# Kernel optimization log

Hardware: AMD Instinct MI355X
Metric: run time of the kernel (lower is better)

Reference implementation:

```python
import jax, jax.numpy as jnp
import numpy as np

EMBED_DIM = 1024
NUM_HEADS = 16
DK = EMBED_DIM // NUM_HEADS  # 64
B, S = 8, 4096


def setup_inputs() -> dict:
    key = jax.random.key(0)
    ks = jax.random.split(key, 7)
    init = 1.0 / np.sqrt(EMBED_DIM)
    x = jax.random.normal(ks[0], (B, S, EMBED_DIM), dtype=jnp.float32)
    Wq = jax.random.uniform(ks[1], (EMBED_DIM, EMBED_DIM), jnp.float32, -init, init)
    bq = jax.random.uniform(ks[2], (EMBED_DIM,), jnp.float32, -init, init)
    Wk = jax.random.uniform(ks[3], (EMBED_DIM, EMBED_DIM), jnp.float32, -init, init)
    bk = jax.random.uniform(ks[4], (EMBED_DIM,), jnp.float32, -init, init)
    Wv = jax.random.uniform(ks[5], (EMBED_DIM, EMBED_DIM), jnp.float32, -init, init)
    bv = jax.random.uniform(ks[6], (EMBED_DIM,), jnp.float32, -init, init)
    return {"x": x, "Wq": Wq, "bq": bq, "Wk": Wk, "bk": bk, "Wv": Wv, "bv": bv}


def reference(x, Wq, bq, Wk, bk, Wv, bv):
    batch_size, seq_length, _ = x.shape
    # Linear projections (torch nn.Linear: x @ W.T + b)
    q = x @ Wq.T + bq  # [B, S, E]
    k = x @ Wk.T + bk
    v = x @ Wv.T + bv
    scaling = 1.0 / jnp.sqrt(jnp.asarray(DK, dtype=x.dtype))
    # Faithful to original: transpose(1,2) then reshape splits heads along the
    # embedding axis -> per-head tensors of shape [B*H, dk, S]
    q = jnp.transpose(q, (0, 2, 1)).reshape(batch_size * NUM_HEADS, DK, seq_length)
    k = jnp.transpose(k, (0, 2, 1)).reshape(batch_size * NUM_HEADS, DK, seq_length)
    k = jnp.transpose(k, (0, 2, 1))  # [B*H, S, dk]
    v = jnp.transpose(v, (0, 2, 1)).reshape(batch_size * NUM_HEADS, DK, seq_length)
    # attn: [B*H, dk, dk] -- attention over channel dims (as in the original code)
    attn = jax.nn.softmax(jnp.einsum('bds,bse->bde', q, k) * scaling, axis=-1)
    output = jnp.einsum('bde,bes->bds', attn, v)  # [B*H, dk, S]
    output = output.reshape(batch_size, EMBED_DIM, seq_length)
    return jnp.transpose(output, (0, 2, 1))  # [B, S, E]
```

## Files before the change

### kernel.cpp

```cpp
#include <hip/hip_runtime.h>
#include <hip/hip_bf16.h>
#include <stdint.h>


#define B_   8
#define S_   4096
#define E_   1024
#define H_   16
#define NSPLIT 4

typedef float floatx4 __attribute__((ext_vector_type(4)));
typedef short short8  __attribute__((ext_vector_type(8)));

#define MFMA(a,b,c) __builtin_amdgcn_mfma_f32_16x16x32_bf16((a),(b),(c),0,0,0)

static __device__ __forceinline__ unsigned short f2bf(float x){
    __hip_bfloat16 h = __float2bfloat16(x);
    return __builtin_bit_cast(unsigned short, h);
}
static __device__ __forceinline__ float bf2f(unsigned short u){
    unsigned int w = ((unsigned int)u) << 16;
    return __builtin_bit_cast(float, w);
}
static __device__ __forceinline__ short8 lds_load8(const unsigned short* p) {
    union { ushort4 u4[2]; short8 s8; } f;
    f.u4[0] = *(const ushort4*)(p);
    f.u4[1] = *(const ushort4*)(p + 4);
    return f.s8;
}
static __device__ __forceinline__ int swz(int chunk, int row){
    return chunk ^ ((row >> 3) & 7) ^ (row & 7);
}
static __device__ __forceinline__ int rk_idx(int row, int col){
    return row * 128 + (((col >> 3) ^ (row & 15)) << 3) + (col & 7);
}
#define SWIZ(row, q) ((q) ^ (((row) >> 1) & 3))

__global__ __launch_bounds__(256) void sums_kernel(
    const float* __restrict__ X, float* __restrict__ cpart, float* __restrict__ d2part)
{
    const int b = blockIdx.y, chunk = blockIdx.z;
    const int e = blockIdx.x * 256 + threadIdx.x;
    const float* p = X + ((size_t)b * S_ + chunk * 256) * E_ + e;
    float s1 = 0.f, s2 = 0.f;
#pragma unroll 8
    for (int i = 0; i < 256; ++i) {
        float v = p[(size_t)i * E_];
        s1 += v; s2 += v * v;
    }
    cpart [(chunk * B_ + b) * E_ + e] = s1;
    d2part[(chunk * B_ + b) * E_ + e] = s2;
}

__global__ __launch_bounds__(256) void reduce_kernel(
    const float* __restrict__ cpart, const float* __restrict__ d2part,
    float* __restrict__ c, float* __restrict__ gdiag)
{
    const int idx = blockIdx.x * 256 + threadIdx.x;
    const int b = idx >> 10, e = idx & 1023;
    float s1 = 0.f, s2 = 0.f;
#pragma unroll
    for (int p = 0; p < 16; ++p) {
        s1 += cpart [(p * B_ + b) * E_ + e];
        s2 += d2part[(p * B_ + b) * E_ + e];
    }
    c[idx] = s1; gdiag[idx] = s2;
}

__global__ __launch_bounds__(256) void uqk_kernel(
    const float* __restrict__ Wq, const float* __restrict__ Wk,
    const float* __restrict__ c, float* __restrict__ uq, float* __restrict__ uk)
{
    const int b = blockIdx.y;
    const int j = blockIdx.x * 256 + threadIdx.x;
    const float* cb = c + b * E_;
    const float* q = Wq + (size_t)j * E_;
    const float* k = Wk + (size_t)j * E_;
    float sq = 0.f, sk = 0.f;
    for (int i = 0; i < E_; i += 4) {
        float4 vq = *(const float4*)(q + i);
        float4 vk = *(const float4*)(k + i);
        float4 cv = *(const float4*)(cb + i);
        sq += vq.x*cv.x + vq.y*cv.y + vq.z*cv.z + vq.w*cv.w;
        sk += vk.x*cv.x + vk.y*cv.y + vk.z*cv.z + vk.w*cv.w;
    }
    uq[b * E_ + j] = sq;
    uk[b * E_ + j] = sk;
}

__global__ __launch_bounds__(256, 4) void gram_kernel(
    const float* __restrict__ X, float* __restrict__ Gp)
{
    const int b = blockIdx.y;
    const int ks = blockIdx.z;
    int u = blockIdx.x, mb = 0;
    while (u >= 8 - mb) { u -= 8 - mb; ++mb; }
    const int nb = mb + u;
    const int m0 = mb * 128, n0 = nb * 128;
    const bool diag = (mb == nb);
    const int t = threadIdx.x, lane = t & 63, w = t >> 6;
    const int l15 = lane & 15, quad = lane >> 4;
    const int mw = 64 * (w >> 1), nw = 64 * (w & 1);
    const int e4 = t & 31, sgrp = t >> 5;

    __shared__ __align__(16) unsigned short At[128 * 64];
    __shared__ __align__(16) unsigned short Bt[128 * 64];

    const floatx4 fz = {0.f, 0.f, 0.f, 0.f};
    floatx4 acc[4][4];
#pragma unroll
    for (int i = 0; i < 4; ++i)
#pragma unroll
        for (int j = 0; j < 4; ++j) acc[i][j] = fz;

    const float* Xb = X + (size_t)b * S_ * E_;
    const int s_begin = ks * (S_ / NSPLIT);
    const int s_end   = s_begin + (S_ / NSPLIT);

    for (int s0 = s_begin; s0 < s_end; s0 += 64) {
        __syncthreads();
#pragma unroll
        for (int p = 0; p < 2; ++p) {
            float4 va[4], vb[4];
#pragma unroll
            for (int i = 0; i < 4; ++i) {
                const int sl = 8 * sgrp + 4 * p + i;
                va[i] = *(const float4*)(Xb + (size_t)(s0 + sl) * E_ + m0 + e4 * 4);
                if (!diag)
                    vb[i] = *(const float4*)(Xb + (size_t)(s0 + sl) * E_ + n0 + e4 * 4);
            }
#pragma unroll
            for (int j = 0; j < 4; ++j) {
                const int e = e4 * 4 + j;
                ushort4 wa;
                wa.x = f2bf(((const float*)&va[0])[j]);
                wa.y = f2bf(((const float*)&va[1])[j]);
                wa.z = f2bf(((const float*)&va[2])[j]);
                wa.w = f2bf(((const float*)&va[3])[j]);
                *(ushort4*)&At[e * 64 + swz(sgrp, e) * 8 + 4 * p] = wa;
                if (!diag) {
                    ushort4 wb;
                    wb.x = f2bf(((const float*)&vb[0])[j]);
                    wb.y = f2bf(((const float*)&vb[1])[j]);
                    wb.z = f2bf(((const float*)&vb[2])[j]);
                    wb.w = f2bf(((const float*)&vb[3])[j]);
                    *(ushort4*)&Bt[e * 64 + swz(sgrp, e) * 8 + 4 * p] = wb;
                }
            }
        }
        __syncthreads();
        const unsigned short* Bp = diag ? At : Bt;
#pragma unroll
        for (int kk = 0; kk < 2; ++kk) {
            const int q = kk * 4 + quad;
            short8 af[4], bfr[4];
#pragma unroll
            for (int i = 0; i < 4; ++i) {
                const int row = mw + 16 * i + l15;
                af[i] = lds_load8(&At[row * 64 + swz(q, row) * 8]);
            }
#pragma unroll
            for (int j = 0; j < 4; ++j) {
                const int row = nw + 16 * j + l15;
                bfr[j] = lds_load8(&Bp[row * 64 + swz(q, row) * 8]);
            }
#pragma unroll
            for (int i = 0; i < 4; ++i)
#pragma unroll
                for (int j = 0; j < 4; ++j)
                    acc[i][j] = MFMA(af[i], bfr[j], acc[i][j]);
        }
    }

    float* Gb = Gp + ((size_t)ks * B_ + b) * E_ * E_;
#pragma unroll
    for (int jt = 0; jt < 4; ++jt)
#pragma unroll
        for (int i = 0; i < 4; ++i)
#pragma unroll
            for (int r = 0; r < 4; ++r) {
                const int row = mw + 16 * i + quad * 4 + r;
                const int col = nw + 16 * jt + l15;
                const float v = acc[i][jt][r];
                Gb[(size_t)(m0 + row) * E_ + n0 + col] = v;
                if (!diag) Gb[(size_t)(n0 + col) * E_ + m0 + row] = v;
            }
}

__global__ __launch_bounds__(256) void greduce_kernel(float* __restrict__ Gp)
{
    const size_t n = (size_t)B_ * E_ * E_;
    const size_t i = ((size_t)blockIdx.x * 256 + threadIdx.x) * 4;
    float4 v0 = *(const float4*)(Gp + i);
    float4 v1 = *(const float4*)(Gp + n + i);
    float4 v2 = *(const float4*)(Gp + 2 * n + i);
    float4 v3 = *(const float4*)(Gp + 3 * n + i);
    float4 r = { v0.x + v1.x + v2.x + v3.x,
                 v0.y + v1.y + v2.y + v3.y,
                 v0.z + v1.z + v2.z + v3.z,
                 v0.w + v1.w + v2.w + v3.w };
    *(float4*)(Gp + i) = r;
}

__global__ __launch_bounds__(256) void z_kernel(
    const float* __restrict__ G, const float* __restrict__ WqF,
    const float* __restrict__ gdiag, float* __restrict__ Z)
{
    const int b = blockIdx.z;
    const int n0 = blockIdx.x * 128;
    const int m0 = blockIdx.y * 128;
    const int t = threadIdx.x, lane = t & 63, w = t >> 6;
    const int l15 = lane & 15, quad = lane >> 4;
    const int mw = 64 * (w >> 1), nw = 64 * (w & 1);

    __shared__ __align__(16) unsigned short As[128 * 32];
    __shared__ __align__(16) unsigned short Bs[128 * 32];

    const float* Gb = G + (size_t)b * E_ * E_;
    const float* gd = gdiag + b * E_;
    float* Zb = Z + (size_t)b * E_ * E_;

    const floatx4 fz = {0.f, 0.f, 0.f, 0.f};
    floatx4 acc[4][4];
#pragma unroll
    for (int i = 0; i < 4; ++i)
#pragma unroll
        for (int j = 0; j < 4; ++j) acc[i][j] = fz;

    for (int k0 = 0; k0 < E_; k0 += 32) {
        __syncthreads();
#pragma unroll
        for (int it = 0; it < 4; ++it) {
            const int l = t + 256 * it;
            const int c4 = l & 7, row = l >> 3;
            float4 v = *(const float4*)(WqF + (size_t)(m0 + row) * E_ + k0 + c4 * 4);
            ushort4 o = { f2bf(v.x), f2bf(v.y), f2bf(v.z), f2bf(v.w) };
            *(ushort4*)&As[row * 32 + SWIZ(row, c4 >> 1) * 8 + (c4 & 1) * 4] = o;
        }
#pragma unroll
        for (int it = 0; it < 4; ++it) {
            const int l = t + 256 * it;
            const int c4 = l & 7, row = l >> 3;
            const int n = n0 + row;
            float4 v = *(const float4*)(Gb + (size_t)n * E_ + k0 + c4 * 4);
            float vv[4] = {v.x, v.y, v.z, v.w};
            const int dj = n - (k0 + c4 * 4);
            if (dj >= 0 && dj < 4) vv[dj] = 0.f;
            ushort4 o = { f2bf(vv[0]), f2bf(vv[1]), f2bf(vv[2]), f2bf(vv[3]) };
            *(ushort4*)&Bs[row * 32 + SWIZ(row, c4 >> 1) * 8 + (c4 & 1) * 4] = o;
        }
        __syncthreads();
        short8 af[4], bfr[4];
#pragma unroll
        for (int i = 0; i < 4; ++i) {
            const int row = mw + 16 * i + l15;
            af[i] = lds_load8(&As[row * 32 + SWIZ(row, quad) * 8]);
        }
#pragma unroll
        for (int j = 0; j < 4; ++j) {
            const int row = nw + 16 * j + l15;
            bfr[j] = lds_load8(&Bs[row * 32 + SWIZ(row, quad) * 8]);
        }
#pragma unroll
        for (int i = 0; i < 4; ++i)
#pragma unroll
            for (int j = 0; j < 4; ++j)
                acc[i][j] = MFMA(af[i], bfr[j], acc[i][j]);
    }

#pragma unroll
    for (int jt = 0; jt < 4; ++jt) {
        const int n = n0 + nw + 16 * jt + l15;
        const float g = gd[n];
#pragma unroll
        for (int i = 0; i < 4; ++i)
#pragma unroll
            for (int r = 0; r < 4; ++r) {
                const int m = m0 + mw + 16 * i + quad * 4 + r;
                Zb[(size_t)m * E_ + n] = acc[i][jt][r] + WqF[(size_t)m * E_ + n] * g;
            }
    }
}

__global__ __launch_bounds__(256) void attn_kernel(
    const float* __restrict__ Z,
    const float* __restrict__ bqF,
    const float* __restrict__ WkF, const float* __restrict__ bkF,
    const float* __restrict__ WvF, const float* __restrict__ bvF,
    const float* __restrict__ uq, const float* __restrict__ uk,
    unsigned short* __restrict__ Wo, float* __restrict__ bo)
{
    const int bh = blockIdx.x, b = bh >> 4, h = bh & 15;
    const int t = threadIdx.x, lane = t & 63, w = t >> 6;
    const int l15 = lane & 15, quad = lane >> 4;

    __shared__ __align__(16) unsigned char smem[65536];
    unsigned short* ZH  = (unsigned short*)(smem);
    unsigned short* ZL  = (unsigned short*)(smem + 16384);
    unsigned short* KH  = (unsigned short*)(smem + 32768);
    unsigned short* KL  = (unsigned short*)(smem + 49152);
    unsigned short* PB  = (unsigned short*)(smem);
    unsigned short* WVT = (unsigned short*)(smem + 16384);

    const float* Zh  = Z   + ((size_t)b * E_ + h * 64) * E_;
    const float* Wkh = WkF + (size_t)(h * 64) * E_;
    const float* Wvh = WvF + (size_t)(h * 64) * E_;

    const floatx4 fz = {0.f, 0.f, 0.f, 0.f};
    floatx4 lacc[4] = {fz, fz, fz, fz};

    for (int ic = 0; ic < 8; ++ic) {
        __syncthreads();
#pragma unroll
        for (int it = 0; it < 8; ++it) {
            const int l = t + 256 * it;
            const int c4 = l & 31, row = l >> 5;
            float4 v = *(const float4*)(Zh + (size_t)row * E_ + ic * 128 + c4 * 4);
            const float vv[4] = {v.x, v.y, v.z, v.w};
            ushort4 ohi, olo;
#pragma unroll
            for (int j = 0; j < 4; ++j) {
                const unsigned short hi = f2bf(vv[j]);
                ((unsigned short*)&ohi)[j] = hi;
                ((unsigned short*)&olo)[j] = f2bf(vv[j] - bf2f(hi));
            }
            const int off = row * 128 + (((c4 >> 1) ^ (row & 15)) << 3) + (c4 & 1) * 4;
            *(ushort4*)&ZH[off] = ohi;
            *(ushort4*)&ZL[off] = olo;
        }
#pragma unroll
        for (int it = 0; it < 8; ++it) {
            const int l = t + 256 * it;
            const int c4 = l & 31, row = l >> 5;
            float4 v = *(const float4*)(Wkh + (size_t)row * E_ + ic * 128 + c4 * 4);
            const float vv[4] = {v.x, v.y, v.z, v.w};
            ushort4 ohi, olo;
#pragma unroll
            for (int j = 0; j < 4; ++j) {
                const unsigned short hi = f2bf(vv[j]);
                ((unsigned short*)&ohi)[j] = hi;
                ((unsigned short*)&olo)[j] = f2bf(vv[j] - bf2f(hi));
            }
            const int off = row * 128 + (((c4 >> 1) ^ (row & 15)) << 3) + (c4 & 1) * 4;
            *(ushort4*)&KH[off] = ohi;
            *(ushort4*)&KL[off] = olo;
        }
        __syncthreads();
#pragma unroll
        for (int ks = 0; ks < 4; ++ks) {
            const short8 ah = lds_load8(&ZH[rk_idx(16 * w + l15, ks * 32 + quad * 8)]);
            const short8 al = lds_load8(&ZL[rk_idx(16 * w + l15, ks * 32 + quad * 8)]);
#pragma unroll
            for (int jt = 0; jt < 4; ++jt) {
                const short8 bh_ = lds_load8(&KH[rk_idx(16 * jt + l15, ks * 32 + quad * 8)]);
                const short8 bl_ = lds_load8(&KL[rk_idx(16 * jt + l15, ks * 32 + quad * 8)]);
                lacc[jt] = MFMA(ah, bh_, lacc[jt]);
                lacc[jt] = MFMA(ah, bl_, lacc[jt]);
                lacc[jt] = MFMA(al, bh_, lacc[jt]);
            }
        }
    }

    float ukv[4], bkv[4];
#pragma unroll
    for (int jt = 0; jt < 4; ++jt) {
        const int he = h * 64 + 16 * jt + l15;
        ukv[jt] = uk[b * E_ + he];
        bkv[jt] = bkF[he];
    }
    float L[4][4];
#pragma unroll
    for (int r = 0; r < 4; ++r) {
        const int hd = h * 64 + 16 * w + quad * 4 + r;
        const float uqr = uq[b * E_ + hd];
        const float bqr = bqF[hd];
#pragma unroll
        for (int jt = 0; jt < 4; ++jt)
            L[jt][r] = 0.125f * (lacc[jt][r] + bqr * ukv[jt] + bkv[jt] * uqr
                                 + 4096.f * bqr * bkv[jt]);
    }
#pragma unroll
    for (int r = 0; r < 4; ++r) {
        float m = fmaxf(fmaxf(L[0][r], L[1][r]), fmaxf(L[2][r], L[3][r]));
#pragma unroll
        for (int mask = 1; mask < 16; mask <<= 1) m = fmaxf(m, __shfl_xor(m, mask, 64));
        float s = 0.f;
#pragma unroll
        for (int jt = 0; jt < 4; ++jt) { L[jt][r] = __expf(L[jt][r] - m); s += L[jt][r]; }
#pragma unroll
        for (int mask = 1; mask < 16; mask <<= 1) s += __shfl_xor(s, mask, 64);
        const float inv = 1.f / s;
#pragma unroll
        for (int jt = 0; jt < 4; ++jt) L[jt][r] *= inv;
    }

    __syncthreads();
#pragma unroll
    for (int jt = 0; jt < 4; ++jt)
#pragma unroll
        for (int r = 0; r < 4; ++r)
            PB[(16 * w + quad * 4 + r) * 72 + 16 * jt + l15] = f2bf(L[jt][r]);
    __syncthreads();

    if (t < 64) {
        float s = 0.f;
        for (int e = 0; e < 64; ++e) s += bf2f(PB[t * 72 + e]) * bvF[h * 64 + e];
        bo[b * E_ + h * 64 + t] = s;
    }

    unsigned short* Wob = Wo + (size_t)b * E_ * E_;
    for (int nc = 0; nc < 16; ++nc) {
        __syncthreads();
#pragma unroll
        for (int it = 0; it < 4; ++it) {
            const int l = t + 256 * it;
            const int n4 = l & 15, e = l >> 4;
            float4 v = *(const float4*)(Wvh + (size_t)e * E_ + nc * 64 + n4 * 4);
            const float vv[4] = {v.x, v.y, v.z, v.w};
#pragma unroll
            for (int j = 0; j < 4; ++j) {
                const int n = n4 * 4 + j;
                WVT[n * 64 + swz(e >> 3, n) * 8 + (e & 7)] = f2bf(vv[j]);
            }
        }
        __syncthreads();
        floatx4 oacc[4] = {fz, fz, fz, fz};
#pragma unroll
        for (int ks = 0; ks < 2; ++ks) {
            const short8 a = lds_load8(&PB[(16 * w + l15) * 72 + ks * 32 + quad * 8]);
            const int q = ks * 4 + quad;
#pragma unroll
            for (int jt = 0; jt < 4; ++jt) {
                const int row = 16 * jt + l15;
                const short8 bb = lds_load8(&WVT[row * 64 + swz(q, row) * 8]);
                oacc[jt] = MFMA(a, bb, oacc[jt]);
            }
        }
#pragma unroll
        for (int jt = 0; jt < 4; ++jt)
#pragma unroll
            for (int r = 0; r < 4; ++r)
                Wob[(size_t)(h * 64 + 16 * w + quad * 4 + r) * E_ + nc * 64 + 16 * jt + l15]
                    = f2bf(oacc[jt][r]);
    }
}

__global__ __launch_bounds__(256) void out_gemm_kernel(
    const float* __restrict__ X, const unsigned short* __restrict__ Wo,
    const float* __restrict__ bo, float* __restrict__ Out)
{
    const int b = blockIdx.z;
    const int n0 = blockIdx.x * 128;
    const int m0 = blockIdx.y * 128;
    const int t = threadIdx.x, lane = t & 63, w = t >> 6;
    const int l15 = lane & 15, quad = lane >> 4;
    const int mw = 64 * (w >> 1), nw = 64 * (w & 1);

    __shared__ __align__(16) unsigned short As[128 * 32];
    __shared__ __align__(16) unsigned short Bs[128 * 32];

    const float* Xb = X + (size_t)b * S_ * E_;
    const unsigned short* Wb = Wo + (size_t)b * E_ * E_;
    const float* bob = bo + b * E_;
    float* Ob = Out + (size_t)b * S_ * E_;

    const floatx4 fz = {0.f, 0.f, 0.f, 0.f};
    floatx4 acc[4][4];
#pragma unroll
    for (int i = 0; i < 4; ++i)
#pragma unroll
        for (int j = 0; j < 4; ++j) acc[i][j] = fz;

    for (int k0 = 0; k0 < E_; k0 += 32) {
        __syncthreads();
#pragma unroll
        for (int it = 0; it < 4; ++it) {
            const int l = t + 256 * it;
            const int c4 = l & 7, row = l >> 3;
            float4 v = *(const float4*)(Xb + (size_t)(m0 + row) * E_ + k0 + c4 * 4);
            ushort4 o = { f2bf(v.x), f2bf(v.y), f2bf(v.z), f2bf(v.w) };
            *(ushort4*)&As[row * 32 + SWIZ(row, c4 >> 1) * 8 + (c4 & 1) * 4] = o;
        }
#pragma unroll
        for (int it = 0; it < 2; ++it) {
            const int l = t + 256 * it;
            const int ch = l & 3, row = l >> 2;
            uint4 v = *(const uint4*)(Wb + (size_t)(n0 + row) * E_ + k0 + ch * 8);
            *(uint4*)&Bs[row * 32 + SWIZ(row, ch) * 8] = v;
        }
        __syncthreads();
        short8 af[4], bfr[4];
#pragma unroll
        for (int i = 0; i < 4; ++i) {
            const int row = mw + 16 * i + l15;
            af[i] = lds_load8(&As[row * 32 + SWIZ(row, quad) * 8]);
        }
#pragma unroll
        for (int j = 0; j < 4; ++j) {
            const int row = nw + 16 * j + l15;
            bfr[j] = lds_load8(&Bs[row * 32 + SWIZ(row, quad) * 8]);
        }
#pragma unroll
        for (int i = 0; i < 4; ++i)
#pragma unroll
            for (int j = 0; j < 4; ++j)
                acc[i][j] = MFMA(af[i], bfr[j], acc[i][j]);
    }

#pragma unroll
    for (int jt = 0; jt < 4; ++jt) {
        const int n = n0 + nw + 16 * jt + l15;
        const float bv_ = bob[n];
        float* colp = Ob + n;
#pragma unroll
        for (int i = 0; i < 4; ++i)
#pragma unroll
            for (int r = 0; r < 4; ++r) {
                const int m = m0 + mw + 16 * i + quad * 4 + r;
                colp[(size_t)m * E_] = acc[i][jt][r] + bv_;
            }
    }
}

extern "C" void kernel_launch(void* const* d_in, const int* in_sizes, int n_in,
                              void* d_out, int out_size, void* d_ws, size_t ws_size,
                              hipStream_t stream) {
    (void)in_sizes; (void)n_in; (void)out_size; (void)ws_size;
    const float* x  = (const float*)d_in[0];
    const float* Wq = (const float*)d_in[1];
    const float* bq = (const float*)d_in[2];
    const float* Wk = (const float*)d_in[3];
    const float* bk = (const float*)d_in[4];
    const float* Wv = (const float*)d_in[5];
    const float* bv = (const float*)d_in[6];

    unsigned short* Wo = (unsigned short*)d_ws;
    float* cpart  = (float*)(Wo + (size_t)B_ * E_ * E_);
    float* d2part = cpart  + 16 * B_ * E_;
    float* c      = d2part + 16 * B_ * E_;
    float* gdiag  = c      + B_ * E_;
    float* uq     = gdiag  + B_ * E_;
    float* uk     = uq     + B_ * E_;
    float* bo     = uk     + B_ * E_;

    float* Gp = (float*)d_out;
    float* G  = Gp;
    float* Z  = Gp + (size_t)B_ * E_ * E_;

    sums_kernel<<<dim3(4, 8, 16), 256, 0, stream>>>(x, cpart, d2part);
    reduce_kernel<<<dim3(32), 256, 0, stream>>>(cpart, d2part, c, gdiag);
    uqk_kernel<<<dim3(4, 8), 256, 0, stream>>>(Wq, Wk, c, uq, uk);
    gram_kernel<<<dim3(36, 8, NSPLIT), 256, 0, stream>>>(x, Gp);
    greduce_kernel<<<dim3(8192), 256, 0, stream>>>(Gp);
    z_kernel<<<dim3(8, 8, 8), 256, 0, stream>>>(G, Wq, gdiag, Z);
    attn_kernel<<<dim3(128), 256, 0, stream>>>(Z, bq, Wk, bk, Wv, bv,
                                               uq, uk, Wo, bo);
    out_gemm_kernel<<<dim3(8, 32, 8), 256, 0, stream>>>(x, Wo, bo, (float*)d_out);
}
```

Measured before the change: 765.9 us.

## Add register prefetch pipelining and XCD-aware block remapping across GEMM kernels

The gram kernel switches to a 32-wide K step with double-buffered LDS and register prefetch of the next X tile, so global loads overlap the MFMA work. The z and attn kernels gain the same prefetch of the next tile into registers. The gram, z and out_gemm launches become 1D grids, with block ids remapped so that blocks sharing a batch land on the same XCD for L2 locality. The costs are higher register pressure (gram launch bounds drop to 3 blocks per CU) and more LDS in gram.

```diff
diff --git a/kernel.cpp b/kernel.cpp
--- a/kernel.cpp
+++ b/kernel.cpp
@@ -35,6 +35,7 @@
     return row * 128 + (((col >> 3) ^ (row & 15)) << 3) + (col & 7);
 }
 #define SWIZ(row, q) ((q) ^ (((row) >> 1) & 3))
+#define GSWZ(row, q) ((q) ^ (((row) >> 2) & 3))
 
 __global__ __launch_bounds__(256) void sums_kernel(
     const float* __restrict__ X, float* __restrict__ cpart, float* __restrict__ d2part)
@@ -88,12 +89,15 @@
     uk[b * E_ + j] = sk;
 }
 
-__global__ __launch_bounds__(256, 4) void gram_kernel(
+__global__ __launch_bounds__(256, 3) void gram_kernel(
     const float* __restrict__ X, float* __restrict__ Gp)
 {
-    const int b = blockIdx.y;
-    const int ks = blockIdx.z;
-    int u = blockIdx.x, mb = 0;
+    const int bid = blockIdx.x;
+    const int v = (bid & 7) * 144 + (bid >> 3);
+    const int g = v / 36;
+    int u = v - g * 36;
+    const int b = g >> 2, ks = g & 3;
+    int mb = 0;
     while (u >= 8 - mb) { u -= 8 - mb; ++mb; }
     const int nb = mb + u;
     const int m0 = mb * 128, n0 = nb * 128;
@@ -101,10 +105,10 @@
     const int t = threadIdx.x, lane = t & 63, w = t >> 6;
     const int l15 = lane & 15, quad = lane >> 4;
     const int mw = 64 * (w >> 1), nw = 64 * (w & 1);
-    const int e4 = t & 31, sgrp = t >> 5;
-
-    __shared__ __align__(16) unsigned short At[128 * 64];
-    __shared__ __align__(16) unsigned short Bt[128 * 64];
+    const int e4 = t & 31, sg = t >> 5;
+
+    __shared__ __align__(16) unsigned short At[2][128 * 32];
+    __shared__ __align__(16) unsigned short Bt[2][128 * 32];
 
     const floatx4 fz = {0.f, 0.f, 0.f, 0.f};
     floatx4 acc[4][4];
@@ -117,59 +121,53 @@
     const int s_begin = ks * (S_ / NSPLIT);
     const int s_end   = s_begin + (S_ / NSPLIT);
 
-    for (int s0 = s_begin; s0 < s_end; s0 += 64) {
-        __syncthreads();
-#pragma unroll
-        for (int p = 0; p < 2; ++p) {
-            float4 va[4], vb[4];
-#pragma unroll
-            for (int i = 0; i < 4; ++i) {
-                const int sl = 8 * sgrp + 4 * p + i;
-                va[i] = *(const float4*)(Xb + (size_t)(s0 + sl) * E_ + m0 + e4 * 4);
-                if (!diag)
-                    vb[i] = *(const float4*)(Xb + (size_t)(s0 + sl) * E_ + n0 + e4 * 4);
-            }
-#pragma unroll
-            for (int j = 0; j < 4; ++j) {
-                const int e = e4 * 4 + j;
-                ushort4 wa;
-                wa.x = f2bf(((const float*)&va[0])[j]);
-                wa.y = f2bf(((const float*)&va[1])[j]);
-                wa.z = f2bf(((const float*)&va[2])[j]);
-                wa.w = f2bf(((const float*)&va[3])[j]);
-                *(ushort4*)&At[e * 64 + swz(sgrp, e) * 8 + 4 * p] = wa;
-                if (!diag) {
-                    ushort4 wb;
-                    wb.x = f2bf(((const float*)&vb[0])[j]);
-                    wb.y = f2bf(((const float*)&vb[1])[j]);
-                    wb.z = f2bf(((const float*)&vb[2])[j]);
-                    wb.w = f2bf(((const float*)&vb[3])[j]);
-                    *(ushort4*)&Bt[e * 64 + swz(sgrp, e) * 8 + 4 * p] = wb;
-                }
-            }
-        }
-        __syncthreads();
-        const unsigned short* Bp = diag ? At : Bt;
-#pragma unroll
-        for (int kk = 0; kk < 2; ++kk) {
-            const int q = kk * 4 + quad;
-            short8 af[4], bfr[4];
-#pragma unroll
-            for (int i = 0; i < 4; ++i) {
-                const int row = mw + 16 * i + l15;
-                af[i] = lds_load8(&At[row * 64 + swz(q, row) * 8]);
-            }
-#pragma unroll
-            for (int j = 0; j < 4; ++j) {
-                const int row = nw + 16 * j + l15;
-                bfr[j] = lds_load8(&Bp[row * 64 + swz(q, row) * 8]);
-            }
-#pragma unroll
-            for (int i = 0; i < 4; ++i)
-#pragma unroll
-                for (int j = 0; j < 4; ++j)
-                    acc[i][j] = MFMA(af[i], bfr[j], acc[i][j]);
-        }
+    float4 pa[4], pb[4];
+    auto gload = [&](int s0) {
+#pragma unroll
+        for (int i = 0; i < 4; ++i) {
+            const float* rp = Xb + (size_t)(s0 + 4 * sg + i) * E_;
+            pa[i] = *(const float4*)(rp + m0 + e4 * 4);
+            if (!diag) pb[i] = *(const float4*)(rp + n0 + e4 * 4);
+        }
+    };
+
+    gload(s_begin);
+    int cur = 0;
+    for (int s0 = s_begin; s0 < s_end; s0 += 32) {
+#pragma unroll
+        for (int j = 0; j < 4; ++j) {
+            const int e = e4 * 4 + j;
+            const int off = e * 32 + (GSWZ(e, sg >> 1) << 3) + (sg & 1) * 4;
+            ushort4 wa = { f2bf(((const float*)&pa[0])[j]), f2bf(((const float*)&pa[1])[j]),
+                           f2bf(((const float*)&pa[2])[j]), f2bf(((const float*)&pa[3])[j]) };
+            *(ushort4*)&At[cur][off] = wa;
+            if (!diag) {
+                ushort4 wb = { f2bf(((const float*)&pb[0])[j]), f2bf(((const float*)&pb[1])[j]),
+                               f2bf(((const float*)&pb[2])[j]), f2bf(((const float*)&pb[3])[j]) };
+                *(ushort4*)&Bt[cur][off] = wb;
+            }
+        }
+        if (s0 + 32 < s_end) gload(s0 + 32);
+        __syncthreads();
+        const unsigned short* Ap = At[cur];
+        const unsigned short* Bq = diag ? At[cur] : Bt[cur];
+        short8 af[4], bfr[4];
+#pragma unroll
+        for (int i = 0; i < 4; ++i) {
+            const int row = mw + 16 * i + l15;
+            af[i] = lds_load8(&Ap[row * 32 + (GSWZ(row, quad) << 3)]);
+        }
+#pragma unroll
+        for (int j = 0; j < 4; ++j) {
+            const int row = nw + 16 * j + l15;
+            bfr[j] = lds_load8(&Bq[row * 32 + (GSWZ(row, quad) << 3)]);
+        }
+#pragma unroll
+        for (int i = 0; i < 4; ++i)
+#pragma unroll
+            for (int j = 0; j < 4; ++j)
+                acc[i][j] = MFMA(af[i], bfr[j], acc[i][j]);
+        cur ^= 1;
     }
 
     float* Gb = Gp + ((size_t)ks * B_ + b) * E_ * E_;
@@ -181,9 +179,9 @@
             for (int r = 0; r < 4; ++r) {
                 const int row = mw + 16 * i + quad * 4 + r;
                 const int col = nw + 16 * jt + l15;
-                const float v = acc[i][jt][r];
-                Gb[(size_t)(m0 + row) * E_ + n0 + col] = v;
-                if (!diag) Gb[(size_t)(n0 + col) * E_ + m0 + row] = v;
+                const float v2 = acc[i][jt][r];
+                Gb[(size_t)(m0 + row) * E_ + n0 + col] = v2;
+                if (!diag) Gb[(size_t)(n0 + col) * E_ + m0 + row] = v2;
             }
 }
 
@@ -206,12 +204,15 @@
     const float* __restrict__ G, const float* __restrict__ WqF,
     const float* __restrict__ gdiag, float* __restrict__ Z)
 {
-    const int b = blockIdx.z;
-    const int n0 = blockIdx.x * 128;
-    const int m0 = blockIdx.y * 128;
+    const int bid = blockIdx.x;
+    const int b = bid & 7;
+    const int rem = bid >> 3;
+    const int n0 = (rem & 7) * 128;
+    const int m0 = (rem >> 3) * 128;
     const int t = threadIdx.x, lane = t & 63, w = t >> 6;
     const int l15 = lane & 15, quad = lane >> 4;
     const int mw = 64 * (w >> 1), nw = 64 * (w & 1);
+    const int c4 = t & 7, srow = t >> 3;
 
     __shared__ __align__(16) unsigned short As[128 * 32];
     __shared__ __align__(16) unsigned short Bs[128 * 32];
@@ -227,28 +228,33 @@
 #pragma unroll
         for (int j = 0; j < 4; ++j) acc[i][j] = fz;
 
+    float4 qa[4], gb4[4];
+    auto zload = [&](int k0) {
+#pragma unroll
+        for (int it = 0; it < 4; ++it) {
+            const int row = srow + 32 * it;
+            qa[it]  = *(const float4*)(WqF + (size_t)(m0 + row) * E_ + k0 + c4 * 4);
+            gb4[it] = *(const float4*)(Gb  + (size_t)(n0 + row) * E_ + k0 + c4 * 4);
+        }
+    };
+
+    zload(0);
     for (int k0 = 0; k0 < E_; k0 += 32) {
         __syncthreads();
 #pragma unroll
         for (int it = 0; it < 4; ++it) {
-            const int l = t + 256 * it;
-            const int c4 = l & 7, row = l >> 3;
-            float4 v = *(const float4*)(WqF + (size_t)(m0 + row) * E_ + k0 + c4 * 4);
-            ushort4 o = { f2bf(v.x), f2bf(v.y), f2bf(v.z), f2bf(v.w) };
-            *(ushort4*)&As[row * 32 + SWIZ(row, c4 >> 1) * 8 + (c4 & 1) * 4] = o;
-        }
-#pragma unroll
-        for (int it = 0; it < 4; ++it) {
-            const int l = t + 256 * it;
-            const int c4 = l & 7, row = l >> 3;
+            const int row = srow + 32 * it;
+            const int off = row * 32 + SWIZ(row, c4 >> 1) * 8 + (c4 & 1) * 4;
+            ushort4 oa = { f2bf(qa[it].x), f2bf(qa[it].y), f2bf(qa[it].z), f2bf(qa[it].w) };
+            *(ushort4*)&As[off] = oa;
             const int n = n0 + row;
-            float4 v = *(const float4*)(Gb + (size_t)n * E_ + k0 + c4 * 4);
-            float vv[4] = {v.x, v.y, v.z, v.w};
+            float vv[4] = {gb4[it].x, gb4[it].y, gb4[it].z, gb4[it].w};
             const int dj = n - (k0 + c4 * 4);
             if (dj >= 0 && dj < 4) vv[dj] = 0.f;
-            ushort4 o = { f2bf(vv[0]), f2bf(vv[1]), f2bf(vv[2]), f2bf(vv[3]) };
-            *(ushort4*)&Bs[row * 32 + SWIZ(row, c4 >> 1) * 8 + (c4 & 1) * 4] = o;
-        }
+            ushort4 ob = { f2bf(vv[0]), f2bf(vv[1]), f2bf(vv[2]), f2bf(vv[3]) };
+            *(ushort4*)&Bs[off] = ob;
+        }
+        if (k0 + 32 < E_) zload(k0 + 32);
         __syncthreads();
         short8 af[4], bfr[4];
 #pragma unroll
@@ -271,13 +277,13 @@
 #pragma unroll
     for (int jt = 0; jt < 4; ++jt) {
         const int n = n0 + nw + 16 * jt + l15;
-        const float g = gd[n];
+        const float gdi = gd[n];
 #pragma unroll
         for (int i = 0; i < 4; ++i)
 #pragma unroll
             for (int r = 0; r < 4; ++r) {
                 const int m = m0 + mw + 16 * i + quad * 4 + r;
-                Zb[(size_t)m * E_ + n] = acc[i][jt][r] + WqF[(size_t)m * E_ + n] * g;
+                Zb[(size_t)m * E_ + n] = acc[i][jt][r] + WqF[(size_t)m * E_ + n] * gdi;
             }
     }
 }
@@ -309,42 +315,51 @@
     const floatx4 fz = {0.f, 0.f, 0.f, 0.f};
     floatx4 lacc[4] = {fz, fz, fz, fz};
 
-    for (int ic = 0; ic < 8; ++ic) {
-        __syncthreads();
+    float4 zv[8], kv[8];
+    auto aload = [&](int ic) {
 #pragma unroll
         for (int it = 0; it < 8; ++it) {
             const int l = t + 256 * it;
-            const int c4 = l & 31, row = l >> 5;
-            float4 v = *(const float4*)(Zh + (size_t)row * E_ + ic * 128 + c4 * 4);
-            const float vv[4] = {v.x, v.y, v.z, v.w};
-            ushort4 ohi, olo;
-#pragma unroll
-            for (int j = 0; j < 4; ++j) {
-                const unsigned short hi = f2bf(vv[j]);
-                ((unsigned short*)&ohi)[j] = hi;
-                ((unsigned short*)&olo)[j] = f2bf(vv[j] - bf2f(hi));
-            }
-            const int off = row * 128 + (((c4 >> 1) ^ (row & 15)) << 3) + (c4 & 1) * 4;
-            *(ushort4*)&ZH[off] = ohi;
-            *(ushort4*)&ZL[off] = olo;
-        }
+            const int cc = l & 31, row = l >> 5;
+            zv[it] = *(const float4*)(Zh  + (size_t)row * E_ + ic * 128 + cc * 4);
+            kv[it] = *(const float4*)(Wkh + (size_t)row * E_ + ic * 128 + cc * 4);
+        }
+    };
+
+    aload(0);
+    for (int ic = 0; ic < 8; ++ic) {
+        __syncthreads();
 #pragma unroll
         for (int it = 0; it < 8; ++it) {
             const int l = t + 256 * it;
-            const int c4 = l & 31, row = l >> 5;
-            float4 v = *(const float4*)(Wkh + (size_t)row * E_ + ic * 128 + c4 * 4);
-            const float vv[4] = {v.x, v.y, v.z, v.w};
-            ushort4 ohi, olo;
-#pragma unroll
-            for (int j = 0; j < 4; ++j) {
-                const unsigned short hi = f2bf(vv[j]);
-                ((unsigned short*)&ohi)[j] = hi;
-                ((unsigned short*)&olo)[j] = f2bf(vv[j] - bf2f(hi));
-            }
-            const int off = row * 128 + (((c4 >> 1) ^ (row & 15)) << 3) + (c4 & 1) * 4;
-            *(ushort4*)&KH[off] = ohi;
-            *(ushort4*)&KL[off] = olo;
-        }
+            const int cc = l & 31, row = l >> 5;
+            const int off = row * 128 + (((cc >> 1) ^ (row & 15)) << 3) + (cc & 1) * 4;
+            {
+                const float vv[4] = {zv[it].x, zv[it].y, zv[it].z, zv[it].w};
+                ushort4 ohi, olo;
+#pragma unroll
+                for (int j = 0; j < 4; ++j) {
+                    const unsigned short hi = f2bf(vv[j]);
+                    ((unsigned short*)&ohi)[j] = hi;
+                    ((unsigned short*)&olo)[j] = f2bf(vv[j] - bf2f(hi));
+                }
+                *(ushort4*)&ZH[off] = ohi;
+                *(ushort4*)&ZL[off] = olo;
+            }
+            {
+                const float vv[4] = {kv[it].x, kv[it].y, kv[it].z, kv[it].w};
+                ushort4 ohi, olo;
+#pragma unroll
+                for (int j = 0; j < 4; ++j) {
+                    const unsigned short hi = f2bf(vv[j]);
+                    ((unsigned short*)&ohi)[j] = hi;
+                    ((unsigned short*)&olo)[j] = f2bf(vv[j] - bf2f(hi));
+                }
+                *(ushort4*)&KH[off] = ohi;
+                *(ushort4*)&KL[off] = olo;
+            }
+        }
+        if (ic < 7) aload(ic + 1);
         __syncthreads();
 #pragma unroll
         for (int ks = 0; ks < 4; ++ks) {
@@ -449,9 +464,11 @@
     const float* __restrict__ X, const unsigned short* __restrict__ Wo,
     const float* __restrict__ bo, float* __restrict__ Out)
 {
-    const int b = blockIdx.z;
-    const int n0 = blockIdx.x * 128;
-    const int m0 = blockIdx.y * 128;
+    const int bid = blockIdx.x;
+    const int b = bid & 7;
+    const int rem = bid >> 3;
+    const int n0 = (rem & 7) * 128;
+    const int m0 = (rem >> 3) * 128;
     const int t = threadIdx.x, lane = t & 63, w = t >> 6;
     const int l15 = lane & 15, quad = lane >> 4;
     const int mw = 64 * (w >> 1), nw = 64 * (w & 1);
@@ -550,10 +567,10 @@
     sums_kernel<<<dim3(4, 8, 16), 256, 0, stream>>>(x, cpart, d2part);
     reduce_kernel<<<dim3(32), 256, 0, stream>>>(cpart, d2part, c, gdiag);
     uqk_kernel<<<dim3(4, 8), 256, 0, stream>>>(Wq, Wk, c, uq, uk);
-    gram_kernel<<<dim3(36, 8, NSPLIT), 256, 0, stream>>>(x, Gp);
+    gram_kernel<<<dim3(1152), 256, 0, stream>>>(x, Gp);
     greduce_kernel<<<dim3(8192), 256, 0, stream>>>(Gp);
-    z_kernel<<<dim3(8, 8, 8), 256, 0, stream>>>(G, Wq, gdiag, Z);
+    z_kernel<<<dim3(512), 256, 0, stream>>>(G, Wq, gdiag, Z);
     attn_kernel<<<dim3(128), 256, 0, stream>>>(Z, bq, Wk, bk, Wv, bv,
                                                uq, uk, Wo, bo);
-    out_gemm_kernel<<<dim3(8, 32, 8), 256, 0, stream>>>(x, Wo, bo, (float*)d_out);
-}
+    out_gemm_kernel<<<dim3(2048), 256, 0, stream>>>(x, Wo, bo, (float*)d_out);
+}
```

New measurement: 654.3 us. 14.6% less time.
